# Kernel optimization log

Hardware: AMD Instinct MI355X
Metric: run time of the kernel (lower is better)

The kernel has to match this reference:

```python
import jax, jax.numpy as jnp
import numpy as np

EPS = 1e-3  # keras BatchNormalization default epsilon


def _conv1x1(x, W, b):
    # x: (b, h, w, cin), W: (cin, cout)
    return jnp.einsum('bhwc,cd->bhwd', x, W) + b


def _bn(x, gamma, beta, mean, var):
    # inference-mode batch norm (moving statistics)
    return gamma * (x - mean) * jax.lax.rsqrt(var + EPS) + beta


def setup_inputs() -> dict:
    key = jax.random.key(0)
    ks = jax.random.split(key, 20)
    C, Ci = 512, 256
    B, Ha, Wa, Hd, Wd = 8, 32, 32, 64, 64
    s_in = 1.0 / np.sqrt(C)
    s_ic = 1.0 / np.sqrt(Ci)
    inp = {
        'detect': jax.random.normal(ks[0], (B, Hd, Wd, C), jnp.float32),
        'aim': jax.random.normal(ks[1], (B, Ha, Wa, C), jnp.float32),
        # g, theta, phi: C -> Ci 1x1 convs
        'Wg': jax.random.normal(ks[2], (C, Ci), jnp.float32) * s_in,
        'bg': jnp.zeros((Ci,), jnp.float32),
        'Wt': jax.random.normal(ks[3], (C, Ci), jnp.float32) * s_in,
        'bt': jnp.zeros((Ci,), jnp.float32),
        'Wp': jax.random.normal(ks[4], (C, Ci), jnp.float32) * s_in,
        'bp': jnp.zeros((Ci,), jnp.float32),
        # W branch: Ci -> C conv + BN
        'Ww': jax.random.normal(ks[5], (Ci, C), jnp.float32) * s_ic,
        'bw': jnp.zeros((C,), jnp.float32),
        'gw': jnp.ones((C,), jnp.float32),
        'betw': jnp.zeros((C,), jnp.float32),
        'mw': jax.random.normal(ks[6], (C,), jnp.float32) * 0.1,
        'vw': jax.random.uniform(ks[7], (C,), jnp.float32, 0.5, 1.5),
        # Q branch: Ci -> C conv + BN
        'Wq': jax.random.normal(ks[8], (Ci, C), jnp.float32) * s_ic,
        'bq': jnp.zeros((C,), jnp.float32),
        'gq': jnp.ones((C,), jnp.float32),
        'betq': jnp.zeros((C,), jnp.float32),
        'mq': jax.random.normal(ks[9], (C,), jnp.float32) * 0.1,
        'vq': jax.random.uniform(ks[10], (C,), jnp.float32, 0.5, 1.5),
    }
    return inp


def reference(detect, aim, Wg, bg, Wt, bt, Wp, bp,
              Ww, bw, gw, betw, mw, vw,
              Wq, bq, gq, betq, mq, vq):
    B, Ha, Wa, C = aim.shape
    _, Hd, Wd, _ = detect.shape
    Ci = Wg.shape[1]
    Na, Nd = Ha * Wa, Hd * Wd

    d_x = _conv1x1(detect, Wg, bg).reshape(B, Nd, Ci)     # (b, Nd, Ci)
    a_x = _conv1x1(aim, Wg, bg).reshape(B, Na, Ci)        # (b, Na, Ci)
    theta_x = _conv1x1(aim, Wt, bt).reshape(B, Na, Ci)    # (b, Na, Ci)
    phi_x = _conv1x1(detect, Wp, bp).reshape(B, Nd, Ci)   # (b, Nd, Ci)

    # affinity: (b, Na, Nd)
    f = jnp.einsum('bnc,bmc->bnm', theta_x, phi_x)
    f_div_C = f / Nd          # normalize by last dim of f
    fi_div_C = jnp.swapaxes(f, 1, 2) / Na  # (b, Nd, Na), normalized by its last dim

    non_aim = jnp.einsum('bnm,bmc->bnc', f_div_C, d_x).reshape(B, Ha, Wa, Ci)
    non_aim = _bn(_conv1x1(non_aim, Ww, bw), gw, betw, mw, vw) + aim

    non_det = jnp.einsum('bmn,bnc->bmc', fi_div_C, a_x).reshape(B, Hd, Wd, Ci)
    non_det = _bn(_conv1x1(non_det, Wq, bq), gq, betq, mq, vq) + detect

    return non_aim, non_det
```

## Files before the change

kernel.cpp:

```cpp
#include <hip/hip_runtime.h>

typedef unsigned short ushort_t;
typedef unsigned int uint32;
typedef __bf16 bf16x8 __attribute__((ext_vector_type(8)));
typedef float f32x4 __attribute__((ext_vector_type(4)));
typedef uint32 u32x4 __attribute__((ext_vector_type(4)));
typedef uint32 u32x2 __attribute__((ext_vector_type(2)));

typedef __attribute__((address_space(3))) uint32 as3_u32;
typedef const __attribute__((address_space(1))) uint32 as1_u32c;

__device__ __forceinline__ void gl_lds16(const ushort_t* g, ushort_t* l) {
    __builtin_amdgcn_global_load_lds((as1_u32c*)g, (as3_u32*)l, 16, 0, 0);
}

__device__ __forceinline__ float bf2f(ushort_t u) {
    uint32 x = ((uint32)u) << 16;
    return __builtin_bit_cast(float, x);
}
__device__ __forceinline__ ushort_t f2bf(float f) {
    uint32 x = __builtin_bit_cast(uint32, f);
    x += 0x7fffu + ((x >> 16) & 1u);
    return (ushort_t)(x >> 16);
}
__device__ __forceinline__ void ld4bf(const ushort_t* p, float* f) {
    const u32x2 w = *(const u32x2*)p;
    f[0] = bf2f((ushort_t)(w[0] & 0xffffu)); f[1] = bf2f((ushort_t)(w[0] >> 16));
    f[2] = bf2f((ushort_t)(w[1] & 0xffffu)); f[3] = bf2f((ushort_t)(w[1] >> 16));
}
__device__ __forceinline__ u32x2 pk4bf(const float* v) {
    u32x2 pk;
    pk[0] = (uint32)f2bf(v[0]) | ((uint32)f2bf(v[1]) << 16);
    pk[1] = (uint32)f2bf(v[2]) | ((uint32)f2bf(v[3]) << 16);
    return pk;
}

struct VecArgs { const void* s[14]; ushort_t* d[14]; int n[14]; };
__global__ void sniff_vec_kernel(const uint32* __restrict__ src, int* __restrict__ flag,
                                 VecArgs a) {
    __shared__ int cnt;
    if (threadIdx.x == 0) cnt = 0;
    __syncthreads();
    if (threadIdx.x < 64) {
        int weird = 0;
        for (int c = 0; c < 4; c++) {
            uint32 w = src[threadIdx.x * 4 + c];
            uint32 e = (w >> 7) & 0xFFu;
            weird += (e < 64u) || (e >= 192u);
        }
        if (weird) atomicAdd(&cnt, weird);
    }
    __syncthreads();
    const bool isf32 = (cnt > 32);
    if (threadIdx.x == 0) *flag = isf32 ? 1 : 0;
    const int t = threadIdx.x;
    for (int seg = 0; seg < 14; seg++) {
        const int n = a.n[seg];
        if (isf32) {
            const float* s = (const float*)a.s[seg];
            for (int i = t; i < n; i += 256) a.d[seg][i] = f2bf(s[i]);
        } else {
            const ushort_t* s = (const ushort_t*)a.s[seg];
            for (int i = t; i < n; i += 256) a.d[seg][i] = s[i];
        }
    }
}

struct WtArgs { const void* s[6]; ushort_t* d[6]; int R[6]; int C[6]; };
__global__ void canon_all(const void* __restrict__ dsrc, ushort_t* __restrict__ ddst,
                          const void* __restrict__ asrc, ushort_t* __restrict__ adst,
                          WtArgs wa, const int* __restrict__ flag) {
    const bool isf32 = (*flag != 0);
    const int b = blockIdx.x;
    if (b < 3072) {
        const void* src; ushort_t* dst; long n; int b0, nb;
        if (b < 2048) { src = dsrc; dst = ddst; n = 16777216; b0 = b; nb = 2048; }
        else          { src = asrc; dst = adst; n = 4194304;  b0 = b - 2048; nb = 1024; }
        long i = ((long)b0 * 256 + threadIdx.x) * 8;
        const long stride = (long)nb * 256 * 8;
        if (isf32) {
            const float* s = (const float*)src;
            for (; i < n; i += stride) {
                const f32x4 a = *(const f32x4*)(s + i);
                const f32x4 c = *(const f32x4*)(s + i + 4);
                u32x4 o;
                o[0] = (uint32)f2bf(a[0]) | ((uint32)f2bf(a[1]) << 16);
                o[1] = (uint32)f2bf(a[2]) | ((uint32)f2bf(a[3]) << 16);
                o[2] = (uint32)f2bf(c[0]) | ((uint32)f2bf(c[1]) << 16);
                o[3] = (uint32)f2bf(c[2]) | ((uint32)f2bf(c[3]) << 16);
                *(u32x4*)(dst + i) = o;
            }
        } else {
            const ushort_t* s = (const ushort_t*)src;
            for (; i < n; i += stride)
                *(u32x4*)(dst + i) = *(const u32x4*)(s + i);
        }
    } else {
        const int local = b - 3072;
        const int wsel = local >> 8;
        const int rem = local & 255;
        const int tr = rem >> 4, tc = rem & 15;
        const int R = wa.R[wsel], C = wa.C[wsel];
        if (tc * 32 >= C || tr * 32 >= R) return;
        __shared__ float s[32][33];
        const int t = threadIdx.x;
        const int r = t >> 3, c4 = (t & 7) * 4;
        const long sbase = (long)(tr * 32 + r) * C + tc * 32 + c4;
        if (isf32) {
            const float* S = (const float*)wa.s[wsel];
            const f32x4 v = *(const f32x4*)(S + sbase);
            for (int u = 0; u < 4; u++) s[r][c4 + u] = v[u];
        } else {
            const ushort_t* S = (const ushort_t*)wa.s[wsel];
            for (int u = 0; u < 4; u++) s[r][c4 + u] = bf2f(S[sbase + u]);
        }
        __syncthreads();
        float tv[4];
        for (int u = 0; u < 4; u++) tv[u] = s[c4 + u][r];
        *(u32x2*)(wa.d[wsel] + (long)(tc * 32 + r) * R + tr * 32 + c4) = pk4bf(tv);
    }
}

__global__ void reduce_t2_kernel(const float* __restrict__ P1, const float* __restrict__ P2,
                                 ushort_t* __restrict__ G1T, ushort_t* __restrict__ G2T) {
    __shared__ float s[32][33];
    const int zz = blockIdx.z;
    const float* P = (zz < 8) ? P1 : P2;
    ushort_t* out  = (zz < 8) ? G1T : G2T;
    const int b = zz & 7;
    const int tm = blockIdx.y, tn = blockIdx.x;
    const int t = threadIdx.x;
    const int r = t >> 3, c4 = (t & 7) * 4;
    const float* base = P + (long)b * 8 * 65536 + (long)(tm * 32 + r) * 256 + tn * 32 + c4;
    f32x4 acc = {0.f, 0.f, 0.f, 0.f};
    for (int kc = 0; kc < 8; kc++) acc += *(const f32x4*)(base + (long)kc * 65536);
    for (int u = 0; u < 4; u++) s[r][c4 + u] = acc[u];
    __syncthreads();
    float tv[4];
    for (int u = 0; u < 4; u++) tv[u] = s[c4 + u][r];
    *(u32x2*)(out + (long)b * 65536 + (long)(tn * 32 + r) * 256 + tm * 32 + c4) = pk4bf(tv);
}

#define BM 128
#define BN 128
#define BK 32
#define LDSH (BM * BK)
#define NBUF 3
#define BIGN (1 << 30)

enum { EPI_BIAS = 0, EPI_BIASR = 1, EPI_SCALE = 2, EPI_BN = 3, EPI_PART = 4 };

struct GP {
    const ushort_t* A; const ushort_t* B; void* Cv; ushort_t* CT;
    const ushort_t* bias; const ushort_t* gamma; const ushort_t* beta;
    const ushort_t* mean; const ushort_t* var; const ushort_t* res;
    long coff, sA, sB, sC;
    int K, lda, ldb, ldc, cnmax, ldT;
    float alpha;
};
struct GP2 { GP g[2]; };

template <int EPI, bool DYNOUT, bool DUALT, bool SWAP>
__global__ __launch_bounds__(256) void gemm_nt(GP2 ga, int ysplit, int zsplit,
                                               const int* __restrict__ flag)
{
    __shared__ __align__(16) ushort_t As[NBUF * LDSH];
    __shared__ __align__(16) ushort_t Bs[NBUF * LDSH];

    const bool isf32 = DYNOUT ? (*flag != 0) : false;

    const uint32 gx = gridDim.x, gy = gridDim.y;
    const uint32 nwg = gx * gy * gridDim.z;
    const uint32 lid = blockIdx.x + gx * (blockIdx.y + gy * blockIdx.z);
    const uint32 swz = (lid & 7u) * (nwg >> 3) + (lid >> 3);
    const uint32 bx = swz % gx, t1 = swz / gx;
    int by = (int)(t1 % gy), bz = (int)(t1 / gy);

    int sel = 0;
    if (by >= ysplit) { by -= ysplit; sel = 1; }
    if (bz >= zsplit) { bz -= zsplit; sel = 1; }
    const GP& p = ga.g[sel];

    const ushort_t* A = p.A + (long)bz * p.sA;
    const ushort_t* B = p.B + (long)bz * p.sB;
    const long cbase = p.coff + (long)bz * p.sC;
    const int lda = p.lda, ldb = p.ldb, ldc = p.ldc, K = p.K;

    const int tid  = threadIdx.x;
    const int lane = tid & 63;
    const int w    = tid >> 6;
    const int wr   = w >> 1, wc = w & 1;
    const int lr   = lane & 15, q = lane >> 4;

    const int m0 = by * BM;
    const int n0 = bx * BN;

    const int lrow = lane >> 2, lu = lane & 3;
    const int us = (lu ^ ((lrow >> 1) & 3)) * 8;
    const int ra0 = w * 32 + lrow, ra1 = w * 32 + 16 + lrow;
    const ushort_t* Ar0 = A + (long)(m0 + ra0) * lda + us;
    const ushort_t* Ar1 = A + (long)(m0 + ra1) * lda + us;
    const ushort_t* Br0 = B + (long)(n0 + ra0) * ldb + us;
    const ushort_t* Br1 = B + (long)(n0 + ra1) * ldb + us;
    ushort_t* sA0 = &As[(w * 2 + 0) * 512];
    ushort_t* sA1 = &As[(w * 2 + 1) * 512];
    ushort_t* sB0 = &Bs[(w * 2 + 0) * 512];
    ushort_t* sB1 = &Bs[(w * 2 + 1) * 512];

    const int swq = (q ^ ((lr >> 1) & 3)) * 8;

    f32x4 acc[4][4];
#pragma unroll
    for (int i = 0; i < 4; i++)
#pragma unroll
        for (int j = 0; j < 4; j++) acc[i][j] = (f32x4){0.f, 0.f, 0.f, 0.f};

    const int nt = K / BK;

    {
        gl_lds16(Ar0, sA0); gl_lds16(Ar1, sA1);
        gl_lds16(Br0, sB0); gl_lds16(Br1, sB1);
        if (nt > 1) {
            gl_lds16(Ar0 + BK, sA0 + LDSH); gl_lds16(Ar1 + BK, sA1 + LDSH);
            gl_lds16(Br0 + BK, sB0 + LDSH); gl_lds16(Br1 + BK, sB1 + LDSH);
        }
    }

    int c0 = 0, c2 = 2;
    for (int t = 0; t < nt; ++t) {
        if (t + 1 < nt) asm volatile("s_waitcnt vmcnt(4)" ::: "memory");
        else            asm volatile("s_waitcnt vmcnt(0)" ::: "memory");
        __builtin_amdgcn_s_barrier();
        __builtin_amdgcn_sched_barrier(0);

        if (t + 2 < nt) {
            const int nb = c2 * LDSH;
            const int kn = (t + 2) * BK;
            gl_lds16(Ar0 + kn, sA0 + nb); gl_lds16(Ar1 + kn, sA1 + nb);
            gl_lds16(Br0 + kn, sB0 + nb); gl_lds16(Br1 + kn, sB1 + nb);
        }
        __builtin_amdgcn_sched_barrier(0);

        const ushort_t* Ab = As + c0 * LDSH;
        const ushort_t* Bb = Bs + c0 * LDSH;
        bf16x8 af[4], bfr[4];
#pragma unroll
        for (int i = 0; i < 4; i++)
            af[i] = __builtin_bit_cast(bf16x8,
                *(const u32x4*)(&Ab[(wr * 64 + i * 16 + lr) * BK + swq]));
#pragma unroll
        for (int j = 0; j < 4; j++)
            bfr[j] = __builtin_bit_cast(bf16x8,
                *(const u32x4*)(&Bb[(wc * 64 + j * 16 + lr) * BK + swq]));
#pragma unroll
        for (int i = 0; i < 4; i++)
#pragma unroll
            for (int j = 0; j < 4; j++) {
                if constexpr (SWAP)
                    acc[i][j] = __builtin_amdgcn_mfma_f32_16x16x32_bf16(bfr[j], af[i], acc[i][j], 0, 0, 0);
                else
                    acc[i][j] = __builtin_amdgcn_mfma_f32_16x16x32_bf16(af[i], bfr[j], acc[i][j], 0, 0, 0);
            }
        __builtin_amdgcn_sched_barrier(0);

        c0 = (c0 + 1 == NBUF) ? 0 : c0 + 1;
        c2 = (c2 + 1 == NBUF) ? 0 : c2 + 1;
    }

    if constexpr (SWAP) {
#pragma unroll
        for (int j = 0; j < 4; j++) {
            const int coln = n0 + wc * 64 + j * 16 + q * 4;
            float sc4[4], sh4[4];
            if constexpr (EPI == EPI_BIAS) {
                float bb[4]; ld4bf(p.bias + coln, bb);
#pragma unroll
                for (int r = 0; r < 4; r++) { sc4[r] = 1.f; sh4[r] = bb[r]; }
            } else if constexpr (EPI == EPI_SCALE) {
#pragma unroll
                for (int r = 0; r < 4; r++) { sc4[r] = p.alpha; sh4[r] = 0.f; }
            } else if constexpr (EPI == EPI_BN) {
                float bb[4], g[4], bt[4], mn[4], vr[4];
                ld4bf(p.bias + coln, bb); ld4bf(p.gamma + coln, g); ld4bf(p.beta + coln, bt);
                ld4bf(p.mean + coln, mn); ld4bf(p.var + coln, vr);
#pragma unroll
                for (int r = 0; r < 4; r++) {
                    const float s = g[r] * rsqrtf(vr[r] + 1e-3f);
                    sc4[r] = s;
                    sh4[r] = s * bb[r] + bt[r] - s * mn[r];
                }
            }
#pragma unroll
            for (int i = 0; i < 4; i++) {
                const int row = m0 + wr * 64 + i * 16 + lr;
                const long off = cbase + (long)row * ldc + coln;
                float v[4];
#pragma unroll
                for (int r = 0; r < 4; r++) v[r] = acc[i][j][r];
                if constexpr (EPI == EPI_BIASR) {
                    const float bs = bf2f(p.bias[row]);
#pragma unroll
                    for (int r = 0; r < 4; r++) v[r] += bs;
                } else if constexpr (EPI == EPI_BN) {
                    float rs[4]; ld4bf(p.res + (long)row * ldc + coln, rs);
#pragma unroll
                    for (int r = 0; r < 4; r++) v[r] = sc4[r] * v[r] + sh4[r] + rs[r];
                } else if constexpr (EPI != EPI_PART) {
#pragma unroll
                    for (int r = 0; r < 4; r++) v[r] = sc4[r] * v[r] + sh4[r];
                }
                if constexpr (EPI == EPI_PART) {
                    *(f32x4*)((float*)p.Cv + off) = (f32x4){v[0], v[1], v[2], v[3]};
                } else if constexpr (DYNOUT) {
                    if (isf32) *(f32x4*)((float*)p.Cv + off) = (f32x4){v[0], v[1], v[2], v[3]};
                    else       *(u32x2*)((ushort_t*)p.Cv + off) = pk4bf(v);
                } else {
                    *(u32x2*)((ushort_t*)p.Cv + off) = pk4bf(v);
                }
            }
        }
    } else {
        const bool doC = (n0 < p.cnmax);
#pragma unroll
        for (int j = 0; j < 4; j++) {
            const int col = n0 + wc * 64 + j * 16 + lr;
            float bs = 0.f, sc = 1.f, sh = 0.f;
            if constexpr (EPI == EPI_BIAS || EPI == EPI_BN) bs = bf2f(p.bias[col]);
            if constexpr (EPI == EPI_BN) {
                const float g  = bf2f(p.gamma[col]);
                const float bt = bf2f(p.beta[col]);
                const float mn = bf2f(p.mean[col]);
                const float vr = bf2f(p.var[col]);
                sc = g * rsqrtf(vr + 1e-3f);
                sh = bt - sc * mn;
            }
#pragma unroll
            for (int i = 0; i < 4; i++) {
                const int rowbase = m0 + wr * 64 + i * 16 + q * 4;
                ushort_t tmp[4];
#pragma unroll
                for (int r = 0; r < 4; r++) {
                    const int row = rowbase + r;
                    float v = acc[i][j][r];
                    if constexpr (EPI == EPI_BIAS) v += bs;
                    else if constexpr (EPI == EPI_BIASR) v += bf2f(p.bias[row]);
                    else if constexpr (EPI == EPI_SCALE) v *= p.alpha;
                    else if constexpr (EPI == EPI_BN)
                        v = sc * (v + bs) + sh + bf2f(p.res[(long)row * ldc + col]);
                    const long off = cbase + (long)row * ldc + col;
                    if constexpr (EPI == EPI_PART) {
                        ((float*)p.Cv)[off] = v;
                    } else if constexpr (DYNOUT) {
                        if (isf32) ((float*)p.Cv)[off] = v;
                        else       ((ushort_t*)p.Cv)[off] = f2bf(v);
                    } else {
                        const ushort_t us2 = f2bf(v);
                        tmp[r] = us2;
                        if (doC) ((ushort_t*)p.Cv)[off] = us2;
                    }
                }
                if constexpr (DUALT) {
                    u32x2 pk;
                    pk[0] = (uint32)tmp[0] | ((uint32)tmp[1] << 16);
                    pk[1] = (uint32)tmp[2] | ((uint32)tmp[3] << 16);
                    *(u32x2*)(p.CT + (long)col * p.ldT + rowbase) = pk;
                }
            }
        }
    }
}

extern "C" void kernel_launch(void* const* d_in, const int* in_sizes, int n_in,
                              void* d_out, int out_size, void* d_ws, size_t ws_size,
                              hipStream_t stream)
{
    int* flag = (int*)d_ws;
    ushort_t* base = (ushort_t*)((char*)d_ws + 16);
    long o = 0;
    ushort_t* detect_c = base + o; o += 16777216;
    ushort_t* aim_c    = base + o; o += 4194304;
    ushort_t* WpgT = base + o; o += 262144;
    ushort_t* WtgT = base + o; o += 262144;
    ushort_t* WwT  = base + o; o += 131072;
    ushort_t* WqT  = base + o; o += 131072;
    ushort_t* bpg_c  = base + o; o += 512;
    ushort_t* btg_c  = base + o; o += 512;
    ushort_t* bw_c   = base + o; o += 512;
    ushort_t* gw_c   = base + o; o += 512;
    ushort_t* betw_c = base + o; o += 512;
    ushort_t* mw_c   = base + o; o += 512;
    ushort_t* vw_c   = base + o; o += 512;
    ushort_t* bq_c   = base + o; o += 512;
    ushort_t* gq_c   = base + o; o += 512;
    ushort_t* betq_c = base + o; o += 512;
    ushort_t* mq_c   = base + o; o += 512;
    ushort_t* vq_c   = base + o; o += 512;
    ushort_t* phi    = base + o; o += 8388608;
    ushort_t* PT     = base + o; o += 16777216;
    ushort_t* theta  = base + o; o += 2097152;
    ushort_t* TT     = base + o; o += 4194304;
    ushort_t* G1T    = base + o; o += 524288;
    ushort_t* G2T    = base + o; o += 524288;
    ushort_t* U      = base + o; o += 16777216;
    float* P1 = (float*)U;
    float* P2 = P1 + 4194304;
    ushort_t* na = U;
    ushort_t* nd = na + 2097152;
    ushort_t* phiT = PT;
    ushort_t* d_xT = PT + 8388608;
    ushort_t* thetaT = TT;
    ushort_t* a_xT = TT + 2097152;

    VecArgs va;
    const int vidx[14] = {7, 3, 5, 3, 9, 10, 11, 12, 13, 15, 16, 17, 18, 19};
    ushort_t* vdst[14] = {bpg_c, bpg_c + 256, btg_c, btg_c + 256,
                          bw_c, gw_c, betw_c, mw_c, vw_c,
                          bq_c, gq_c, betq_c, mq_c, vq_c};
    const int vn[14] = {256, 256, 256, 256, 512, 512, 512, 512, 512, 512, 512, 512, 512, 512};
    for (int i = 0; i < 14; i++) { va.s[i] = d_in[vidx[i]]; va.d[i] = vdst[i]; va.n[i] = vn[i]; }
    sniff_vec_kernel<<<1, 256, 0, stream>>>((const uint32*)d_in[0], flag, va);

    WtArgs wa;
    wa.s[0] = d_in[6];  wa.d[0] = WpgT;              wa.R[0] = 512; wa.C[0] = 256;
    wa.s[1] = d_in[2];  wa.d[1] = WpgT + 256 * 512;  wa.R[1] = 512; wa.C[1] = 256;
    wa.s[2] = d_in[4];  wa.d[2] = WtgT;              wa.R[2] = 512; wa.C[2] = 256;
    wa.s[3] = d_in[2];  wa.d[3] = WtgT + 256 * 512;  wa.R[3] = 512; wa.C[3] = 256;
    wa.s[4] = d_in[8];  wa.d[4] = WwT;               wa.R[4] = 256; wa.C[4] = 512;
    wa.s[5] = d_in[14]; wa.d[5] = WqT;               wa.R[5] = 256; wa.C[5] = 512;
    canon_all<<<4608, 256, 0, stream>>>(d_in[0], detect_c, d_in[1], aim_c, wa, flag);

    const dim3 blk(256);
    const ushort_t* np = nullptr;
    ushort_t* npm = nullptr;

    {
        GP2 g;
        g.g[0] = GP{detect_c, WpgT, phi, PT, bpg_c, np, np, np, np, np,
                    0, 0, 0, 0, 512, 512, 512, 256, 256, 32768, 1.f};
        g.g[1] = GP{aim_c, WtgT, theta, TT, btg_c, np, np, np, np, np,
                    0, 0, 0, 0, 512, 512, 512, 256, 256, 8192, 1.f};
        gemm_nt<EPI_BIAS, false, true, false><<<dim3(4, 320, 1), blk, 0, stream>>>(
            g, 256, BIGN, flag);
    }

    {
        GP2 g;
        g.g[0] = GP{phiT, d_xT, P1, npm, np, np, np, np, np, np,
                    0, 512, 512, 65536, 512, 32768, 32768, 256, BIGN, 0, 1.f};
        g.g[1] = GP{thetaT, a_xT, P2, npm, np, np, np, np, np, np,
                    0, 128, 128, 65536, 128, 8192, 8192, 256, BIGN, 0, 1.f};
        gemm_nt<EPI_PART, false, false, true><<<dim3(2, 2, 128), blk, 0, stream>>>(
            g, BIGN, 64, flag);
    }

    reduce_t2_kernel<<<dim3(8, 8, 16), blk, 0, stream>>>(P1, P2, G1T, G2T);

    {
        GP2 g;
        g.g[0] = GP{phi, G2T, nd, npm, np, np, np, np, np, np,
                    0, 1048576, 65536, 1048576, 256, 256, 256, 256, BIGN, 0, 1.f / 1024.f};
        g.g[1] = GP{theta, G1T, na, npm, np, np, np, np, np, np,
                    0, 262144, 65536, 262144, 256, 256, 256, 256, BIGN, 0, 1.f / 4096.f};
        gemm_nt<EPI_SCALE, false, false, true><<<dim3(2, 40, 8), blk, 0, stream>>>(
            g, 32, BIGN, flag);
    }

    {
        GP2 g;
        g.g[0] = GP{nd, WqT, d_out, npm, bq_c, gq_c, betq_c, mq_c, vq_c, detect_c,
                    8192L * 512, 0, 0, 0, 256, 256, 256, 512, BIGN, 0, 1.f};
        g.g[1] = GP{na, WwT, d_out, npm, bw_c, gw_c, betw_c, mw_c, vw_c, aim_c,
                    0, 0, 0, 0, 256, 256, 256, 512, BIGN, 0, 1.f};
        gemm_nt<EPI_BN, true, false, true><<<dim3(4, 320, 1), blk, 0, stream>>>(
            g, 256, BIGN, flag);
    }
}
```

Measured before the change: 361.9 us.

## Fuse the affinity-apply GEMM with the output conv and BN epilogue

Replaces the separate scale-GEMM (activations times reduced Gram matrix) and the output 1x1 conv+BN GEMM with one kernel. Each block computes a 128x256 intermediate tile, keeps it in swizzled LDS, then multiplies it by the output weights and applies BN plus residual directly. This removes one launch and the global write and re-read of the intermediate na/nd tensors. In exchange, the fused kernel reads operands straight from global memory without LDS staging or pipelining, and it uses 64KB of LDS per block, which may reduce occupancy.

```diff
diff --git a/kernel.cpp b/kernel.cpp
--- a/kernel.cpp
+++ b/kernel.cpp
@@ -216,7 +216,6 @@
         for (int j = 0; j < 4; j++) acc[i][j] = (f32x4){0.f, 0.f, 0.f, 0.f};
 
     const int nt = K / BK;
-
     {
         gl_lds16(Ar0, sA0); gl_lds16(Ar1, sA1);
         gl_lds16(Br0, sB0); gl_lds16(Br1, sB1);
@@ -271,25 +270,6 @@
 #pragma unroll
         for (int j = 0; j < 4; j++) {
             const int coln = n0 + wc * 64 + j * 16 + q * 4;
-            float sc4[4], sh4[4];
-            if constexpr (EPI == EPI_BIAS) {
-                float bb[4]; ld4bf(p.bias + coln, bb);
-#pragma unroll
-                for (int r = 0; r < 4; r++) { sc4[r] = 1.f; sh4[r] = bb[r]; }
-            } else if constexpr (EPI == EPI_SCALE) {
-#pragma unroll
-                for (int r = 0; r < 4; r++) { sc4[r] = p.alpha; sh4[r] = 0.f; }
-            } else if constexpr (EPI == EPI_BN) {
-                float bb[4], g[4], bt[4], mn[4], vr[4];
-                ld4bf(p.bias + coln, bb); ld4bf(p.gamma + coln, g); ld4bf(p.beta + coln, bt);
-                ld4bf(p.mean + coln, mn); ld4bf(p.var + coln, vr);
-#pragma unroll
-                for (int r = 0; r < 4; r++) {
-                    const float s = g[r] * rsqrtf(vr[r] + 1e-3f);
-                    sc4[r] = s;
-                    sh4[r] = s * bb[r] + bt[r] - s * mn[r];
-                }
-            }
 #pragma unroll
             for (int i = 0; i < 4; i++) {
                 const int row = m0 + wr * 64 + i * 16 + lr;
@@ -297,18 +277,6 @@
                 float v[4];
 #pragma unroll
                 for (int r = 0; r < 4; r++) v[r] = acc[i][j][r];
-                if constexpr (EPI == EPI_BIASR) {
-                    const float bs = bf2f(p.bias[row]);
-#pragma unroll
-                    for (int r = 0; r < 4; r++) v[r] += bs;
-                } else if constexpr (EPI == EPI_BN) {
-                    float rs[4]; ld4bf(p.res + (long)row * ldc + coln, rs);
-#pragma unroll
-                    for (int r = 0; r < 4; r++) v[r] = sc4[r] * v[r] + sh4[r] + rs[r];
-                } else if constexpr (EPI != EPI_PART) {
-#pragma unroll
-                    for (int r = 0; r < 4; r++) v[r] = sc4[r] * v[r] + sh4[r];
-                }
                 if constexpr (EPI == EPI_PART) {
                     *(f32x4*)((float*)p.Cv + off) = (f32x4){v[0], v[1], v[2], v[3]};
                 } else if constexpr (DYNOUT) {
@@ -324,16 +292,8 @@
 #pragma unroll
         for (int j = 0; j < 4; j++) {
             const int col = n0 + wc * 64 + j * 16 + lr;
-            float bs = 0.f, sc = 1.f, sh = 0.f;
-            if constexpr (EPI == EPI_BIAS || EPI == EPI_BN) bs = bf2f(p.bias[col]);
-            if constexpr (EPI == EPI_BN) {
-                const float g  = bf2f(p.gamma[col]);
-                const float bt = bf2f(p.beta[col]);
-                const float mn = bf2f(p.mean[col]);
-                const float vr = bf2f(p.var[col]);
-                sc = g * rsqrtf(vr + 1e-3f);
-                sh = bt - sc * mn;
-            }
+            float bs = 0.f;
+            if constexpr (EPI == EPI_BIAS) bs = bf2f(p.bias[col]);
 #pragma unroll
             for (int i = 0; i < 4; i++) {
                 const int rowbase = m0 + wr * 64 + i * 16 + q * 4;
@@ -344,15 +304,9 @@
                     float v = acc[i][j][r];
                     if constexpr (EPI == EPI_BIAS) v += bs;
                     else if constexpr (EPI == EPI_BIASR) v += bf2f(p.bias[row]);
-                    else if constexpr (EPI == EPI_SCALE) v *= p.alpha;
-                    else if constexpr (EPI == EPI_BN)
-                        v = sc * (v + bs) + sh + bf2f(p.res[(long)row * ldc + col]);
                     const long off = cbase + (long)row * ldc + col;
                     if constexpr (EPI == EPI_PART) {
                         ((float*)p.Cv)[off] = v;
-                    } else if constexpr (DYNOUT) {
-                        if (isf32) ((float*)p.Cv)[off] = v;
-                        else       ((ushort_t*)p.Cv)[off] = f2bf(v);
                     } else {
                         const ushort_t us2 = f2bf(v);
                         tmp[r] = us2;
@@ -365,6 +319,133 @@
                     pk[1] = (uint32)tmp[2] | ((uint32)tmp[3] << 16);
                     *(u32x2*)(p.CT + (long)col * p.ldT + rowbase) = pk;
                 }
+            }
+        }
+    }
+}
+
+struct FO {
+    const ushort_t* act; const ushort_t* GT; const ushort_t* W;
+    const ushort_t* bias; const ushort_t* gamma; const ushort_t* beta;
+    const ushort_t* mean; const ushort_t* var; const ushort_t* res;
+    long coff; int bshift; float alpha;
+};
+struct FOArgs { FO f[2]; void* out; };
+
+__device__ __forceinline__ uint32 xswz(int row, int colbyte) {
+    return (uint32)(row * 512 + colbyte) ^ (uint32)((row & 7) << 4);
+}
+
+__global__ __launch_bounds__(256) void fused_out(FOArgs a, const int* __restrict__ flag) {
+    __shared__ __align__(16) ushort_t Xs[128 * 256];
+    const bool isf32 = (*flag != 0);
+
+    const uint32 swz = (blockIdx.x & 7u) * 40u + (blockIdx.x >> 3);
+    const int sel = (swz >= 256u) ? 1 : 0;
+    const int mb = sel ? (int)swz - 256 : (int)swz;
+    const FO p = a.f[sel];
+    const int b = mb >> p.bshift;
+    const ushort_t* A  = p.act + (long)mb * 128 * 256;
+    const ushort_t* GT = p.GT + (long)b * 65536;
+    const ushort_t* res = p.res + (long)mb * 128 * 512;
+    const long cbase = p.coff + (long)mb * 128 * 512;
+
+    const int tid  = threadIdx.x;
+    const int lane = tid & 63;
+    const int w    = tid >> 6;
+    const int wr   = w >> 1, wc = w & 1;
+    const int lr   = lane & 15, q = lane >> 4;
+
+#pragma unroll
+    for (int nh = 0; nh < 2; nh++) {
+        const int n0 = nh * 128;
+        f32x4 acc[4][4];
+#pragma unroll
+        for (int i = 0; i < 4; i++)
+#pragma unroll
+            for (int j = 0; j < 4; j++) acc[i][j] = (f32x4){0.f, 0.f, 0.f, 0.f};
+
+        for (int k0 = 0; k0 < 256; k0 += 32) {
+            bf16x8 af[4], bfr[4];
+#pragma unroll
+            for (int i = 0; i < 4; i++)
+                af[i] = __builtin_bit_cast(bf16x8,
+                    *(const u32x4*)(A + (long)(wr * 64 + i * 16 + lr) * 256 + k0 + q * 8));
+#pragma unroll
+            for (int j = 0; j < 4; j++)
+                bfr[j] = __builtin_bit_cast(bf16x8,
+                    *(const u32x4*)(GT + (long)(n0 + wc * 64 + j * 16 + lr) * 256 + k0 + q * 8));
+#pragma unroll
+            for (int i = 0; i < 4; i++)
+#pragma unroll
+                for (int j = 0; j < 4; j++)
+                    acc[i][j] = __builtin_amdgcn_mfma_f32_16x16x32_bf16(bfr[j], af[i], acc[i][j], 0, 0, 0);
+        }
+#pragma unroll
+        for (int j = 0; j < 4; j++) {
+            const int colb = n0 + wc * 64 + j * 16 + q * 4;
+#pragma unroll
+            for (int i = 0; i < 4; i++) {
+                const int row = wr * 64 + i * 16 + lr;
+                float v[4];
+#pragma unroll
+                for (int r = 0; r < 4; r++) v[r] = acc[i][j][r] * p.alpha;
+                *(u32x2*)((char*)Xs + xswz(row, colb * 2)) = pk4bf(v);
+            }
+        }
+    }
+    __syncthreads();
+
+#pragma unroll 1
+    for (int nb = 0; nb < 4; nb++) {
+        const int n0 = nb * 128;
+        f32x4 acc[4][4];
+#pragma unroll
+        for (int i = 0; i < 4; i++)
+#pragma unroll
+            for (int j = 0; j < 4; j++) acc[i][j] = (f32x4){0.f, 0.f, 0.f, 0.f};
+
+        for (int k0 = 0; k0 < 256; k0 += 32) {
+            bf16x8 af[4], bfr[4];
+#pragma unroll
+            for (int i = 0; i < 4; i++) {
+                const int row = wr * 64 + i * 16 + lr;
+                af[i] = __builtin_bit_cast(bf16x8,
+                    *(const u32x4*)((char*)Xs + xswz(row, (k0 + q * 8) * 2)));
+            }
+#pragma unroll
+            for (int j = 0; j < 4; j++)
+                bfr[j] = __builtin_bit_cast(bf16x8,
+                    *(const u32x4*)(p.W + (long)(n0 + wc * 64 + j * 16 + lr) * 256 + k0 + q * 8));
+#pragma unroll
+            for (int i = 0; i < 4; i++)
+#pragma unroll
+                for (int j = 0; j < 4; j++)
+                    acc[i][j] = __builtin_amdgcn_mfma_f32_16x16x32_bf16(bfr[j], af[i], acc[i][j], 0, 0, 0);
+        }
+
+#pragma unroll
+        for (int j = 0; j < 4; j++) {
+            const int coln = n0 + wc * 64 + j * 16 + q * 4;
+            float bb[4], g[4], bt[4], mn[4], vr[4], sc4[4], sh4[4];
+            ld4bf(p.bias + coln, bb); ld4bf(p.gamma + coln, g); ld4bf(p.beta + coln, bt);
+            ld4bf(p.mean + coln, mn); ld4bf(p.var + coln, vr);
+#pragma unroll
+            for (int r = 0; r < 4; r++) {
+                const float s = g[r] * rsqrtf(vr[r] + 1e-3f);
+                sc4[r] = s;
+                sh4[r] = s * bb[r] + bt[r] - s * mn[r];
+            }
+#pragma unroll
+            for (int i = 0; i < 4; i++) {
+                const int row = wr * 64 + i * 16 + lr;
+                const long off = cbase + (long)row * 512 + coln;
+                float v[4], rs[4];
+                ld4bf(res + (long)row * 512 + coln, rs);
+#pragma unroll
+                for (int r = 0; r < 4; r++) v[r] = sc4[r] * acc[i][j][r] + sh4[r] + rs[r];
+                if (isf32) *(f32x4*)((float*)a.out + off) = (f32x4){v[0], v[1], v[2], v[3]};
+                else       *(u32x2*)((ushort_t*)a.out + off) = pk4bf(v);
             }
         }
     }
@@ -404,8 +485,6 @@
     ushort_t* U      = base + o; o += 16777216;
     float* P1 = (float*)U;
     float* P2 = P1 + 4194304;
-    ushort_t* na = U;
-    ushort_t* nd = na + 2097152;
     ushort_t* phiT = PT;
     ushort_t* d_xT = PT + 8388608;
     ushort_t* thetaT = TT;
@@ -456,22 +535,12 @@
     reduce_t2_kernel<<<dim3(8, 8, 16), blk, 0, stream>>>(P1, P2, G1T, G2T);
 
     {
-        GP2 g;
-        g.g[0] = GP{phi, G2T, nd, npm, np, np, np, np, np, np,
-                    0, 1048576, 65536, 1048576, 256, 256, 256, 256, BIGN, 0, 1.f / 1024.f};
-        g.g[1] = GP{theta, G1T, na, npm, np, np, np, np, np, np,
-                    0, 262144, 65536, 262144, 256, 256, 256, 256, BIGN, 0, 1.f / 4096.f};
-        gemm_nt<EPI_SCALE, false, false, true><<<dim3(2, 40, 8), blk, 0, stream>>>(
-            g, 32, BIGN, flag);
-    }
-
-    {
-        GP2 g;
-        g.g[0] = GP{nd, WqT, d_out, npm, bq_c, gq_c, betq_c, mq_c, vq_c, detect_c,
-                    8192L * 512, 0, 0, 0, 256, 256, 256, 512, BIGN, 0, 1.f};
-        g.g[1] = GP{na, WwT, d_out, npm, bw_c, gw_c, betw_c, mw_c, vw_c, aim_c,
-                    0, 0, 0, 0, 256, 256, 256, 512, BIGN, 0, 1.f};
-        gemm_nt<EPI_BN, true, false, true><<<dim3(4, 320, 1), blk, 0, stream>>>(
-            g, 256, BIGN, flag);
-    }
-}
+        FOArgs fa;
+        fa.out = d_out;
+        fa.f[0] = FO{phi, G2T, WqT, bq_c, gq_c, betq_c, mq_c, vq_c, detect_c,
+                     8192L * 512, 5, 1.f / 1024.f};
+        fa.f[1] = FO{theta, G1T, WwT, bw_c, gw_c, betw_c, mw_c, vw_c, aim_c,
+                     0, 3, 1.f / 4096.f};
+        fused_out<<<320, blk, 0, stream>>>(fa, flag);
+    }
+}
```

Result: slower. 400.8 us (+10.7%).

## Fold per-batch Gram matrix into output projection weights before final GEMM

Applied to the files above, without the earlier changes.

Reassociates the attention chain so that the small per-batch Ci×Ci matrices (phi^T d_x and theta^T a_x, scaled) are first multiplied by the Ww/Wq projection weights. This yields per-batch Ci×C combined matrices, so the separate large GEMM that produced non_aim/non_det intermediates is removed. The final BN GEMM now reads phi/theta directly against these per-batch weights, selected via a new batch shift on the B pointer. The reduce kernel drops its transpose and applies the normalization scale. The BN epilogue branch was removed from the SWAP=false path, and rounding of the folded matrix to bf16 adds extra precision loss.

```diff
diff --git a/kernel.cpp b/kernel.cpp
--- a/kernel.cpp
+++ b/kernel.cpp
@@ -121,24 +121,20 @@
     }
 }
 
-__global__ void reduce_t2_kernel(const float* __restrict__ P1, const float* __restrict__ P2,
-                                 ushort_t* __restrict__ G1T, ushort_t* __restrict__ G2T) {
-    __shared__ float s[32][33];
-    const int zz = blockIdx.z;
+__global__ void reduce_g_kernel(const float* __restrict__ P1, const float* __restrict__ P2,
+                                ushort_t* __restrict__ G1, ushort_t* __restrict__ G2) {
+    const int bxv = blockIdx.x;
+    const int zz = bxv >> 6;
     const float* P = (zz < 8) ? P1 : P2;
-    ushort_t* out  = (zz < 8) ? G1T : G2T;
+    ushort_t* G    = (zz < 8) ? G1 : G2;
+    const float alpha = (zz < 8) ? (1.f / 4096.f) : (1.f / 1024.f);
     const int b = zz & 7;
-    const int tm = blockIdx.y, tn = blockIdx.x;
-    const int t = threadIdx.x;
-    const int r = t >> 3, c4 = (t & 7) * 4;
-    const float* base = P + (long)b * 8 * 65536 + (long)(tm * 32 + r) * 256 + tn * 32 + c4;
+    const long off = ((long)(bxv & 63) * 256 + threadIdx.x) * 4;
+    const float* base = P + (long)b * 8 * 65536 + off;
     f32x4 acc = {0.f, 0.f, 0.f, 0.f};
     for (int kc = 0; kc < 8; kc++) acc += *(const f32x4*)(base + (long)kc * 65536);
-    for (int u = 0; u < 4; u++) s[r][c4 + u] = acc[u];
-    __syncthreads();
-    float tv[4];
-    for (int u = 0; u < 4; u++) tv[u] = s[c4 + u][r];
-    *(u32x2*)(out + (long)b * 65536 + (long)(tn * 32 + r) * 256 + tm * 32 + c4) = pk4bf(tv);
+    float v[4] = {acc[0] * alpha, acc[1] * alpha, acc[2] * alpha, acc[3] * alpha};
+    *(u32x2*)(G + (long)b * 65536 + off) = pk4bf(v);
 }
 
 #define BM 128
@@ -155,7 +151,7 @@
     const ushort_t* bias; const ushort_t* gamma; const ushort_t* beta;
     const ushort_t* mean; const ushort_t* var; const ushort_t* res;
     long coff, sA, sB, sC;
-    int K, lda, ldb, ldc, cnmax, ldT;
+    int K, lda, ldb, ldc, cnmax, ldT, bshift;
     float alpha;
 };
 struct GP2 { GP g[2]; };
@@ -182,7 +178,7 @@
     const GP& p = ga.g[sel];
 
     const ushort_t* A = p.A + (long)bz * p.sA;
-    const ushort_t* B = p.B + (long)bz * p.sB;
+    const ushort_t* B = p.B + ((long)bz + (long)(by >> p.bshift)) * p.sB;
     const long cbase = p.coff + (long)bz * p.sC;
     const int lda = p.lda, ldb = p.ldb, ldc = p.ldc, K = p.K;
 
@@ -216,7 +212,6 @@
         for (int j = 0; j < 4; j++) acc[i][j] = (f32x4){0.f, 0.f, 0.f, 0.f};
 
     const int nt = K / BK;
-
     {
         gl_lds16(Ar0, sA0); gl_lds16(Ar1, sA1);
         gl_lds16(Br0, sB0); gl_lds16(Br1, sB1);
@@ -324,16 +319,8 @@
 #pragma unroll
         for (int j = 0; j < 4; j++) {
             const int col = n0 + wc * 64 + j * 16 + lr;
-            float bs = 0.f, sc = 1.f, sh = 0.f;
-            if constexpr (EPI == EPI_BIAS || EPI == EPI_BN) bs = bf2f(p.bias[col]);
-            if constexpr (EPI == EPI_BN) {
-                const float g  = bf2f(p.gamma[col]);
-                const float bt = bf2f(p.beta[col]);
-                const float mn = bf2f(p.mean[col]);
-                const float vr = bf2f(p.var[col]);
-                sc = g * rsqrtf(vr + 1e-3f);
-                sh = bt - sc * mn;
-            }
+            float bs = 0.f;
+            if constexpr (EPI == EPI_BIAS) bs = bf2f(p.bias[col]);
 #pragma unroll
             for (int i = 0; i < 4; i++) {
                 const int rowbase = m0 + wr * 64 + i * 16 + q * 4;
@@ -345,14 +332,9 @@
                     if constexpr (EPI == EPI_BIAS) v += bs;
                     else if constexpr (EPI == EPI_BIASR) v += bf2f(p.bias[row]);
                     else if constexpr (EPI == EPI_SCALE) v *= p.alpha;
-                    else if constexpr (EPI == EPI_BN)
-                        v = sc * (v + bs) + sh + bf2f(p.res[(long)row * ldc + col]);
                     const long off = cbase + (long)row * ldc + col;
                     if constexpr (EPI == EPI_PART) {
                         ((float*)p.Cv)[off] = v;
-                    } else if constexpr (DYNOUT) {
-                        if (isf32) ((float*)p.Cv)[off] = v;
-                        else       ((ushort_t*)p.Cv)[off] = f2bf(v);
                     } else {
                         const ushort_t us2 = f2bf(v);
                         tmp[r] = us2;
@@ -363,7 +345,7 @@
                     u32x2 pk;
                     pk[0] = (uint32)tmp[0] | ((uint32)tmp[1] << 16);
                     pk[1] = (uint32)tmp[2] | ((uint32)tmp[3] << 16);
-                    *(u32x2*)(p.CT + (long)col * p.ldT + rowbase) = pk;
+                    *(u32x2*)(p.CT + (long)bz * p.sC + (long)col * p.ldT + rowbase) = pk;
                 }
             }
         }
@@ -399,13 +381,13 @@
     ushort_t* PT     = base + o; o += 16777216;
     ushort_t* theta  = base + o; o += 2097152;
     ushort_t* TT     = base + o; o += 4194304;
-    ushort_t* G1T    = base + o; o += 524288;
-    ushort_t* G2T    = base + o; o += 524288;
+    ushort_t* G1     = base + o; o += 524288;
+    ushort_t* G2     = base + o; o += 524288;
+    ushort_t* M1T    = base + o; o += 1048576;
+    ushort_t* M2T    = base + o; o += 1048576;
     ushort_t* U      = base + o; o += 16777216;
     float* P1 = (float*)U;
     float* P2 = P1 + 4194304;
-    ushort_t* na = U;
-    ushort_t* nd = na + 2097152;
     ushort_t* phiT = PT;
     ushort_t* d_xT = PT + 8388608;
     ushort_t* thetaT = TT;
@@ -436,9 +418,9 @@
     {
         GP2 g;
         g.g[0] = GP{detect_c, WpgT, phi, PT, bpg_c, np, np, np, np, np,
-                    0, 0, 0, 0, 512, 512, 512, 256, 256, 32768, 1.f};
+                    0, 0, 0, 0, 512, 512, 512, 256, 256, 32768, 30, 1.f};
         g.g[1] = GP{aim_c, WtgT, theta, TT, btg_c, np, np, np, np, np,
-                    0, 0, 0, 0, 512, 512, 512, 256, 256, 8192, 1.f};
+                    0, 0, 0, 0, 512, 512, 512, 256, 256, 8192, 30, 1.f};
         gemm_nt<EPI_BIAS, false, true, false><<<dim3(4, 320, 1), blk, 0, stream>>>(
             g, 256, BIGN, flag);
     }
@@ -446,31 +428,31 @@
     {
         GP2 g;
         g.g[0] = GP{phiT, d_xT, P1, npm, np, np, np, np, np, np,
-                    0, 512, 512, 65536, 512, 32768, 32768, 256, BIGN, 0, 1.f};
+                    0, 512, 512, 65536, 512, 32768, 32768, 256, BIGN, 0, 30, 1.f};
         g.g[1] = GP{thetaT, a_xT, P2, npm, np, np, np, np, np, np,
-                    0, 128, 128, 65536, 128, 8192, 8192, 256, BIGN, 0, 1.f};
+                    0, 128, 128, 65536, 128, 8192, 8192, 256, BIGN, 0, 30, 1.f};
         gemm_nt<EPI_PART, false, false, true><<<dim3(2, 2, 128), blk, 0, stream>>>(
             g, BIGN, 64, flag);
     }
 
-    reduce_t2_kernel<<<dim3(8, 8, 16), blk, 0, stream>>>(P1, P2, G1T, G2T);
+    reduce_g_kernel<<<1024, blk, 0, stream>>>(P1, P2, G1, G2);
 
     {
         GP2 g;
-        g.g[0] = GP{phi, G2T, nd, npm, np, np, np, np, np, np,
-                    0, 1048576, 65536, 1048576, 256, 256, 256, 256, BIGN, 0, 1.f / 1024.f};
-        g.g[1] = GP{theta, G1T, na, npm, np, np, np, np, np, np,
-                    0, 262144, 65536, 262144, 256, 256, 256, 256, BIGN, 0, 1.f / 4096.f};
-        gemm_nt<EPI_SCALE, false, false, true><<<dim3(2, 40, 8), blk, 0, stream>>>(
-            g, 32, BIGN, flag);
+        g.g[0] = GP{G1, WwT, npm, M1T, np, np, np, np, np, np,
+                    0, 65536, 0, 131072, 256, 256, 256, 512, 0, 256, 30, 1.f};
+        g.g[1] = GP{G2, WqT, npm, M2T, np, np, np, np, np, np,
+                    0, 65536, 0, 131072, 256, 256, 256, 512, 0, 256, 30, 1.f};
+        gemm_nt<EPI_SCALE, false, true, false><<<dim3(4, 2, 16), blk, 0, stream>>>(
+            g, BIGN, 8, flag);
     }
 
     {
         GP2 g;
-        g.g[0] = GP{nd, WqT, d_out, npm, bq_c, gq_c, betq_c, mq_c, vq_c, detect_c,
-                    8192L * 512, 0, 0, 0, 256, 256, 256, 512, BIGN, 0, 1.f};
-        g.g[1] = GP{na, WwT, d_out, npm, bw_c, gw_c, betw_c, mw_c, vw_c, aim_c,
-                    0, 0, 0, 0, 256, 256, 256, 512, BIGN, 0, 1.f};
+        g.g[0] = GP{phi, M2T, d_out, npm, bq_c, gq_c, betq_c, mq_c, vq_c, detect_c,
+                    8192L * 512, 0, 131072, 0, 256, 256, 256, 512, BIGN, 0, 5, 1.f};
+        g.g[1] = GP{theta, M1T, d_out, npm, bw_c, gw_c, betw_c, mw_c, vw_c, aim_c,
+                    0, 0, 131072, 0, 256, 256, 256, 512, BIGN, 0, 3, 1.f};
         gemm_nt<EPI_BN, true, false, true><<<dim3(4, 320, 1), blk, 0, stream>>>(
             g, 256, BIGN, flag);
     }
```

After: 352.4 us. 1.03x faster.
